# Performance work log

Measured on AMD Instinct MI355X. Metric: run time of the kernel, lower is better.

The kernel has to match this reference:

```python
import jax, jax.numpy as jnp
import numpy as np

T, B, I, H, E = 32, 128, 64, 128, 4
N_TRAP = 100  # trapezoid intervals -> 101 sample points


def setup_inputs() -> dict:
    key = jax.random.key(0)
    ks = jax.random.split(key, 14)
    s_cell = 1.0 / np.sqrt(I + H)
    s_wh = 1.0 / np.sqrt((I + H) * E)

    def u(k, shape, s):
        return jax.random.uniform(k, shape, jnp.float32, -s, s)

    return {
        "x_time": jax.random.normal(ks[0], (T, B, I), jnp.float32),
        "dt_time": jax.random.uniform(ks[1], (T, B), jnp.float32, 0.01, 1.0),
        "Wh_w": u(ks[2], ((I + H) * E, H * E), s_wh),
        "Wh_b": u(ks[3], (H * E,), s_wh),
        "Wi_w": u(ks[4], (E, I + H, H), s_cell),
        "Wi_b": u(ks[5], (E, H), s_cell),
        "Wf_w": u(ks[6], (E, I + H, H), s_cell),
        "Wf_b": u(ks[7], (E, H), s_cell),
        "Wd_w": u(ks[8], (E, I + H, H), s_cell),
        "Wd_b": u(ks[9], (E, H), s_cell),
        "Wg_w": u(ks[10], (E, I + H, H), s_cell),
        "Wg_b": u(ks[11], (E, H), s_cell),
        "Wo_w": u(ks[12], (E, I + H, H), s_cell),
        "Wo_b": u(ks[13], (E, H), s_cell),
        "alpha": jnp.ones((E, H), jnp.float32) / H,
    }


def reference(x_time, dt_time, Wh_w, Wh_b, Wi_w, Wi_b, Wf_w, Wf_b,
              Wd_w, Wd_b, Wg_w, Wg_b, Wo_w, Wo_b, alpha):
    t_total, batch, in_dim = x_time.shape
    e_types, hid = alpha.shape
    ts_unit = jnp.linspace(0.0, 1.0, N_TRAP + 1, dtype=x_time.dtype)  # [101]

    def step(carry, inp):
        h, c = carry            # each [E,B,H]
        x, dt = inp             # [B,I], [B]
        # hidden_sum = Wh(cat_m([x, h_m]))
        cat = jnp.concatenate(
            [jnp.concatenate([x, h[m]], axis=-1) for m in range(e_types)], axis=-1)  # [B,(I+H)*E]
        hs = (cat @ Wh_w + Wh_b).reshape(batch, e_types, hid).transpose(1, 0, 2)     # [E,B,H]
        iv = jnp.concatenate(
            [jnp.broadcast_to(x[None], (e_types, batch, in_dim)), hs], axis=-1)       # [E,B,I+H]

        def gate(W, b):
            return jnp.einsum('ebd,edh->ebh', iv, W) + b[:, None, :]

        i_g = jax.nn.sigmoid(gate(Wi_w, Wi_b))
        f_g = jax.nn.sigmoid(gate(Wf_w, Wf_b))
        g = f_g * c + i_g * jnp.tanh(gate(Wg_w, Wg_b))   # curr_g
        delta = jnp.exp(gate(Wd_w, Wd_b))                 # curr_delta
        o = jax.nn.sigmoid(gate(Wo_w, Wo_b))              # curr_o
        diff = c - g                                      # prev_c - curr_g

        c_new = g + diff * jnp.exp(-delta * dt[None, :, None])  # c_t at dt
        h_new = o * jnp.tanh(c_new)
        lam = jnp.einsum('eh,ebh->eb', alpha, h_new)             # intensity at dt

        # trapezoidal integration of intensity over [0, dt], 100 intervals
        ts = dt[:, None] * ts_unit                                # [B,101]
        cv = g[:, :, None, :] + diff[:, :, None, :] * jnp.exp(
            -delta[:, :, None, :] * ts[None, :, :, None])         # [E,B,101,H]
        fv = jnp.einsum('eh,ebth->ebt', alpha, o[:, :, None, :] * jnp.tanh(cv))  # [E,B,101]
        integ = (dt[None, :] / N_TRAP) * (
            jnp.sum(fv, axis=-1) - 0.5 * (fv[..., 0] + fv[..., -1]))  # [E,B]

        return (h_new, c_new), (lam.T, integ.T)  # outputs [B,E]

    h0 = jnp.zeros((e_types, batch, hid), x_time.dtype)
    c0 = jnp.zeros_like(h0)
    _, (lambdas, lambda_integrals) = jax.lax.scan(step, (h0, c0), (x_time, dt_time))
    return lambdas, lambda_integrals  # each [T,B,E]
```

## Files before the change

kernel.cpp:

```cpp
#include <hip/hip_runtime.h>

#define OFF_WALL   0
#define OFF_BIAS   196608
#define OFF_WHHH   199680
#define OFF_WGH    330752
#define OFF_XG     494592
#define OFF_GST    13077504
#define OFF_HBUF   21466112
#define GST_PLANE  2097152
#define H_SENT     0xFFFFFFFFu

typedef _Float16 half2_t __attribute__((ext_vector_type(2)));

__device__ __forceinline__ float fast_sig(float x) {
    return __fdividef(1.f, 1.f + __expf(-x));
}
__device__ __forceinline__ float sig2(float y2) {
    return __builtin_amdgcn_rcpf(exp2f(y2) + 1.f);
}
__device__ __forceinline__ unsigned pack2h(float a, float b) {
    _Float16 ha = (_Float16)a, hb = (_Float16)b;
    unsigned short ua = __builtin_bit_cast(unsigned short, ha);
    unsigned short ub = __builtin_bit_cast(unsigned short, hb);
    return ((unsigned)ub << 16) | ua;
}
__device__ __forceinline__ float dot2(unsigned w, unsigned h, float acc) {
    return __builtin_amdgcn_fdot2(__builtin_bit_cast(half2_t, w),
                                  __builtin_bit_cast(half2_t, h), acc, false);
}

__global__ __launch_bounds__(256) void k0_pack(
    const float* __restrict__ Wh_w, const float* __restrict__ Wh_b,
    const float* __restrict__ Wi_w, const float* __restrict__ Wi_b,
    const float* __restrict__ Wf_w, const float* __restrict__ Wf_b,
    const float* __restrict__ Wd_w, const float* __restrict__ Wd_b,
    const float* __restrict__ Wg_w, const float* __restrict__ Wg_b,
    const float* __restrict__ Wo_w, const float* __restrict__ Wo_b,
    float* __restrict__ ws)
{
    const float* gw[5] = {Wi_w, Wf_w, Wd_w, Wg_w, Wo_w};
    const float* gb[5] = {Wi_b, Wf_b, Wd_b, Wg_b, Wo_b};
    int idx = blockIdx.x * 256 + threadIdx.x;
    if (idx < 196608) {
        int r = idx / 3072, col = idx - r * 3072;
        float v;
        if (col < 512) {
            v = Wh_w[r * 512 + col] + Wh_w[(192 + r) * 512 + col]
              + Wh_w[(384 + r) * 512 + col] + Wh_w[(576 + r) * 512 + col];
        } else {
            int q = col - 512;
            int e = q / 640;
            int rem = q - e * 640;
            int g = rem >> 7, h = rem & 127;
            v = gw[g][(e * 192 + r) * 128 + h];
        }
        ws[OFF_WALL + idx] = v;
    } else if (idx < 327680) {
        int i = idx - 196608;
        int q    = i & 3;
        int lane = (i >> 2) & 127;
        int i4   = (i >> 9) & 15;
        int kq   = (i >> 13) & 3;
        int e    = i >> 15;
        int kp = i4 * 4 + q;
        int k0 = kq * 128 + 2 * kp;
        int r0 = (k0 >> 7) * 192 + 64 + (k0 & 127);
        float w0 = Wh_w[r0 * 512 + e * 128 + lane];
        float w1 = Wh_w[(r0 + 1) * 512 + e * 128 + lane];
        reinterpret_cast<unsigned*>(ws + OFF_WHHH)[i] = pack2h(w0, w1);
    } else if (idx < 491520) {
        int i = idx - 327680;
        int lane = i & 127;
        int gg = (i >> 7) % 5;
        int rest = (i >> 7) / 5;
        int ii = rest & 15;
        int kq = (rest >> 4) & 3;
        int e  = rest >> 6;
        int k0 = kq * 32 + 2 * ii, k1 = k0 + 1;
        float w0 = gw[gg][(e * 192 + 64 + k0) * 128 + lane];
        float w1 = gw[gg][(e * 192 + 64 + k1) * 128 + lane];
        reinterpret_cast<unsigned*>(ws + OFF_WGH)[i] = pack2h(w0, w1);
    }
    if (idx < 3072) {
        float v;
        if (idx < 512) v = Wh_b[idx];
        else {
            int q = idx - 512;
            int e = q / 640;
            int rem = q - e * 640;
            int g = rem >> 7, h = rem & 127;
            v = gb[g][e * 128 + h];
        }
        ws[OFF_BIAS + idx] = v;
    }
    if (idx < 262144) {
        reinterpret_cast<unsigned*>(ws + OFF_HBUF)[idx] = H_SENT;
    }
}

__global__ __launch_bounds__(256) void k1_xproj(
    const float* __restrict__ x, const float* wsr, float* XG)
{
    __shared__ __align__(16) float XT[64 * 68];
    const float* W_all = wsr + OFF_WALL;
    const float* bias  = wsr + OFF_BIAS;
    int bid = blockIdx.x;
    int ct = bid % 48, rt = bid / 48;
    int r0 = rt * 64, c0 = ct * 64;
    for (int p = threadIdx.x; p < 4096; p += 256) {
        int i = p >> 6, k = p & 63;
        XT[k * 68 + i] = x[(r0 + i) * 64 + k];
    }
    __syncthreads();
    int col = c0 + (threadIdx.x & 63);
    int iq = threadIdx.x >> 6;
    float acc[16];
    #pragma unroll
    for (int r = 0; r < 16; r++) acc[r] = 0.f;
    const float* wp = W_all + col;
    #pragma unroll 4
    for (int k = 0; k < 64; k++) {
        float w = wp[k * 3072];
        const float4* xt4 = reinterpret_cast<const float4*>(&XT[k * 68 + iq * 16]);
        #pragma unroll
        for (int r4 = 0; r4 < 4; r4++) {
            float4 xv = xt4[r4];
            acc[r4 * 4 + 0] = fmaf(xv.x, w, acc[r4 * 4 + 0]);
            acc[r4 * 4 + 1] = fmaf(xv.y, w, acc[r4 * 4 + 1]);
            acc[r4 * 4 + 2] = fmaf(xv.z, w, acc[r4 * 4 + 2]);
            acc[r4 * 4 + 3] = fmaf(xv.w, w, acc[r4 * 4 + 3]);
        }
    }
    float bv = bias[col];
    #pragma unroll
    for (int r = 0; r < 16; r++) {
        int row = r0 + iq * 16 + r;
        XG[row * 3072 + col] = acc[r] + bv;
    }
}

__global__ __launch_bounds__(512, 1) void k2_recur(
    const uint4* __restrict__ WhhH4,
    const unsigned* __restrict__ WgH,
    const float* __restrict__ XG,
    const float* __restrict__ dt_time,
    const float* __restrict__ alpha,
    float* __restrict__ Gst,
    unsigned* __restrict__ hbuf,
    float* __restrict__ lam_out)
{
    __shared__ __align__(16) uint4 waL[8192];
    __shared__ __align__(16) unsigned hL[256][2];
    __shared__ __align__(16) unsigned hsP[2][64];
    __shared__ __align__(16) unsigned hOut[128];
    __shared__ float pA[4][2][128];
    __shared__ __align__(16) float pBn[4][2][128][6];
    __shared__ float red[4];
    const int tid = threadIdx.x;
    const int bid = blockIdx.x;
    const int e   = (bid >> 3) & 3;
    const int grp = (bid & 7) | ((bid >> 5) << 3);
    const int b0  = grp * 2;
    const int kq  = tid >> 7;
    const int lane = tid & 127;
    const int l64 = tid & 63;
    const int s = (tid >> 7) & 1, l = lane;

    {
        const uint4* src = WhhH4 + (size_t)e * 8192;
        #pragma unroll
        for (int n = 0; n < 16; ++n) waL[tid + 512 * n] = src[tid + 512 * n];
    }
    unsigned wg[5][16];
    #pragma unroll
    for (int i = 0; i < 16; i++) {
        #pragma unroll
        for (int g = 0; g < 5; g++)
            wg[g][i] = WgH[(((e * 4 + kq) * 16 + i) * 5 + g) * 128 + lane];
    }
    const float av = alpha[e * 128 + lane];
    float cst = 0.f;
    __syncthreads();

    for (int t = 0; t < 32; ++t) {
        const int row0 = t * 128 + b0;
        float xg0 = 0.f, xgg0 = 0.f, xgg1 = 0.f, xgg2 = 0.f, xgg3 = 0.f, xgg4 = 0.f;
        if (tid < 256) {
            const float* base = XG + (size_t)(row0 + s) * 3072;
            xg0 = base[e * 128 + l];
            const float* gp = base + 512 + e * 640 + l;
            xgg0 = gp[0]; xgg1 = gp[128]; xgg2 = gp[256]; xgg3 = gp[384]; xgg4 = gp[512];
        }
        if (t > 0) {
            {
                const int eh = tid >> 7, sh = (tid >> 6) & 1, p = tid & 63;
                unsigned v;
                if (eh == e) {
                    v = hOut[tid & 127];
                } else {
                    unsigned* ap = hbuf + ((size_t)((t & 1) * 64 + grp) * 4 + e) * 512 + tid;
                    v = __hip_atomic_load(ap, __ATOMIC_RELAXED, __HIP_MEMORY_SCOPE_AGENT);
                    while (v == H_SENT) {
                        __builtin_amdgcn_s_sleep(1);
                        v = __hip_atomic_load(ap, __ATOMIC_RELAXED, __HIP_MEMORY_SCOPE_AGENT);
                    }
                    __hip_atomic_store(ap, H_SENT, __ATOMIC_RELAXED,
                                       __HIP_MEMORY_SCOPE_AGENT);
                }
                hL[eh * 64 + p][sh] = v;
            }
            __syncthreads();
            float a0 = 0.f, a1 = 0.f;
            {
                uint2 hu = reinterpret_cast<const uint2*>(hL)[kq * 64 + l64];
                #pragma unroll
                for (int i4 = 0; i4 < 16; ++i4) {
                    uint4 w = waL[(kq * 16 + i4) * 128 + lane];
                    unsigned h0, h1;
                    h0 = __builtin_amdgcn_readlane(hu.x, i4 * 4 + 0);
                    h1 = __builtin_amdgcn_readlane(hu.y, i4 * 4 + 0);
                    a0 = dot2(w.x, h0, a0); a1 = dot2(w.x, h1, a1);
                    h0 = __builtin_amdgcn_readlane(hu.x, i4 * 4 + 1);
                    h1 = __builtin_amdgcn_readlane(hu.y, i4 * 4 + 1);
                    a0 = dot2(w.y, h0, a0); a1 = dot2(w.y, h1, a1);
                    h0 = __builtin_amdgcn_readlane(hu.x, i4 * 4 + 2);
                    h1 = __builtin_amdgcn_readlane(hu.y, i4 * 4 + 2);
                    a0 = dot2(w.z, h0, a0); a1 = dot2(w.z, h1, a1);
                    h0 = __builtin_amdgcn_readlane(hu.x, i4 * 4 + 3);
                    h1 = __builtin_amdgcn_readlane(hu.y, i4 * 4 + 3);
                    a0 = dot2(w.w, h0, a0); a1 = dot2(w.w, h1, a1);
                }
            }
            pA[kq][0][lane] = a0;
            pA[kq][1][lane] = a1;
            __syncthreads();
        }
        if (tid < 256) {
            float hs = xg0;
            if (t > 0) hs += pA[0][s][l] + pA[1][s][l] + pA[2][s][l] + pA[3][s][l];
            float hi = __shfl_down(hs, 1, 64);
            if ((l & 1) == 0) hsP[s][l >> 1] = pack2h(hs, hi);
        }
        __syncthreads();
        float b0a = 0.f, b1a = 0.f, b2a = 0.f, b3a = 0.f, b4a = 0.f;
        float b0b = 0.f, b1b = 0.f, b2b = 0.f, b3b = 0.f, b4b = 0.f;
        {
            unsigned hv = hsP[(l64 >> 4) & 1][kq * 16 + (l64 & 15)];
            #pragma unroll
            for (int i = 0; i < 16; ++i) {
                unsigned h0 = __builtin_amdgcn_readlane(hv, i);
                unsigned h1 = __builtin_amdgcn_readlane(hv, 16 + i);
                b0a = dot2(wg[0][i], h0, b0a); b0b = dot2(wg[0][i], h1, b0b);
                b1a = dot2(wg[1][i], h0, b1a); b1b = dot2(wg[1][i], h1, b1b);
                b2a = dot2(wg[2][i], h0, b2a); b2b = dot2(wg[2][i], h1, b2b);
                b3a = dot2(wg[3][i], h0, b3a); b3b = dot2(wg[3][i], h1, b3b);
                b4a = dot2(wg[4][i], h0, b4a); b4b = dot2(wg[4][i], h1, b4b);
            }
        }
        {
            float2 w01, w23;
            w01.x = b0a; w01.y = b1a; w23.x = b2a; w23.y = b3a;
            *reinterpret_cast<float2*>(&pBn[kq][0][lane][0]) = w01;
            *reinterpret_cast<float2*>(&pBn[kq][0][lane][2]) = w23;
            pBn[kq][0][lane][4] = b4a;
            w01.x = b0b; w01.y = b1b; w23.x = b2b; w23.y = b3b;
            *reinterpret_cast<float2*>(&pBn[kq][1][lane][0]) = w01;
            *reinterpret_cast<float2*>(&pBn[kq][1][lane][2]) = w23;
            pBn[kq][1][lane][4] = b4b;
        }
        __syncthreads();
        if (tid < 256) {
            float ai = xgg0, af = xgg1, ad = xgg2, ag = xgg3, ao = xgg4;
            #pragma unroll
            for (int q = 0; q < 4; ++q) {
                float2 p01 = *reinterpret_cast<const float2*>(&pBn[q][s][l][0]);
                float2 p23 = *reinterpret_cast<const float2*>(&pBn[q][s][l][2]);
                float p4 = pBn[q][s][l][4];
                ai += p01.x; af += p01.y; ad += p23.x; ag += p23.y; ao += p4;
            }
            float ig = fast_sig(ai);
            float fg = fast_sig(af);
            float dl = __expf(ad);
            float gt = tanhf(ag);
            float og = fast_sig(ao);
            float gc = fmaf(fg, cst, ig * gt);
            float df = cst - gc;
            float dtv = dt_time[row0 + s];
            cst = fmaf(df, __expf(-dl * dtv), gc);
            float hn = og * tanhf(cst);
            size_t go = (size_t)(row0 + s) * 512 + e * 128 + l;
            Gst[0 * GST_PLANE + go] = gc;
            Gst[1 * GST_PLANE + go] = df;
            Gst[2 * GST_PLANE + go] = dl;
            Gst[3 * GST_PLANE + go] = og;
            float hi = __shfl_down(hn, 1, 64);
            if ((l & 1) == 0) hOut[s * 64 + (l >> 1)] = pack2h(hn, hi);
            float lm = av * hn;
            #pragma unroll
            for (int off = 32; off > 0; off >>= 1) lm += __shfl_down(lm, off, 64);
            if ((tid & 63) == 0) red[tid >> 6] = lm;
        }
        __syncthreads();
        if (tid == 0) {
            lam_out[(row0 + 0) * 4 + e] = red[0] + red[1];
            lam_out[(row0 + 1) * 4 + e] = red[2] + red[3];
        }
        {
            const int copy = tid >> 7;
            if (copy != e) {
                unsigned* dst = hbuf
                    + ((size_t)(((t + 1) & 1) * 64 + grp) * 4 + copy) * 512
                    + e * 128 + (tid & 127);
                __hip_atomic_store(dst, hOut[tid & 127], __ATOMIC_RELAXED,
                                   __HIP_MEMORY_SCOPE_AGENT);
            }
        }
    }
}

__global__ __launch_bounds__(256) void k3_trap(
    const float* __restrict__ Gst, const float* __restrict__ dt_time,
    const float* __restrict__ alpha, float* __restrict__ integ_out)
{
    __shared__ float red[4][2];
    const int row = blockIdx.x;
    const int tid = threadIdx.x;
    const float dtv = dt_time[row];
    const int base = row * 512;
    const float L2E = 1.4426950408889634f;
    float accv[2];
    #pragma unroll 1
    for (int u = 0; u < 2; ++u) {
        const int p = tid + u * 256;
        float gc = Gst[0 * GST_PLANE + base + p];
        float df = Gst[1 * GST_PLANE + base + p];
        float dl = Gst[2 * GST_PLANE + base + p];
        float o  = Gst[3 * GST_PLANE + base + p];
        float ao = alpha[p] * o;
        float G = 2.f * gc * L2E, D = 2.f * df * L2E;
        float q  = dl * dtv;
        float r1 = exp2f(-q * (0.01f * L2E));
        float r2 = r1 * r1, r4 = r2 * r2;
        float E100 = exp2f(-q * L2E);
        float sE = 0.5f * sig2(G + D) - 0.5f * sig2(fmaf(D, E100, G));
        float E1 = r1, E2 = r2, E3 = r2 * r1, E4 = r4;
        float s1 = 0.f, s2 = 0.f, s3 = 0.f, s4 = 0.f;
        #pragma unroll
        for (int k = 0; k < 25; ++k) {
            s1 += sig2(fmaf(D, E1, G)); E1 *= r4;
            s2 += sig2(fmaf(D, E2, G)); E2 *= r4;
            s3 += sig2(fmaf(D, E3, G)); E3 *= r4;
            s4 += sig2(fmaf(D, E4, G)); E4 *= r4;
        }
        sE += (s1 + s2) + (s3 + s4);
        accv[u] = ao * (100.f - 2.f * sE);
    }
    float vA = accv[0], vB = accv[1];
    #pragma unroll
    for (int off = 32; off > 0; off >>= 1) {
        vA += __shfl_down(vA, off, 64);
        vB += __shfl_down(vB, off, 64);
    }
    const int wv = tid >> 6;
    if ((tid & 63) == 0) { red[wv][0] = vA; red[wv][1] = vB; }
    __syncthreads();
    if (tid < 4) {
        float v = (tid < 2) ? (red[2 * tid][0] + red[2 * tid + 1][0])
                            : (red[2 * (tid - 2)][1] + red[2 * (tid - 2) + 1][1]);
        integ_out[row * 4 + tid] = v * (dtv * 0.01f);
    }
}

extern "C" void kernel_launch(void* const* d_in, const int* in_sizes, int n_in,
                              void* d_out, int out_size, void* d_ws, size_t ws_size,
                              hipStream_t stream)
{
    const float* x_time  = (const float*)d_in[0];
    const float* dt_time = (const float*)d_in[1];
    const float* Wh_w = (const float*)d_in[2];
    const float* Wh_b = (const float*)d_in[3];
    const float* Wi_w = (const float*)d_in[4];
    const float* Wi_b = (const float*)d_in[5];
    const float* Wf_w = (const float*)d_in[6];
    const float* Wf_b = (const float*)d_in[7];
    const float* Wd_w = (const float*)d_in[8];
    const float* Wd_b = (const float*)d_in[9];
    const float* Wg_w = (const float*)d_in[10];
    const float* Wg_b = (const float*)d_in[11];
    const float* Wo_w = (const float*)d_in[12];
    const float* Wo_b = (const float*)d_in[13];
    const float* alpha = (const float*)d_in[14];

    float* ws = (float*)d_ws;
    float* XG   = ws + OFF_XG;
    float* Gst  = ws + OFF_GST;
    unsigned* hbuf = (unsigned*)(ws + OFF_HBUF);
    float* lam_out   = (float*)d_out;
    float* integ_out = lam_out + 32 * 128 * 4;

    k0_pack<<<3072, 256, 0, stream>>>(Wh_w, Wh_b, Wi_w, Wi_b, Wf_w, Wf_b,
                                      Wd_w, Wd_b, Wg_w, Wg_b, Wo_w, Wo_b, ws);
    k1_xproj<<<3072, 256, 0, stream>>>(x_time, ws, XG);
    k2_recur<<<256, 512, 0, stream>>>(
        (const uint4*)(ws + OFF_WHHH), (const unsigned*)(ws + OFF_WGH),
        XG, dt_time, alpha, Gst, hbuf, lam_out);
    k3_trap<<<4096, 256, 0, stream>>>(Gst, dt_time, alpha, integ_out);
}
```

Before: 239.8 us.

## Load remote hidden state directly to registers with 64-bit handoff, reorganize gate reductions

In the recurrent kernel, each thread now reads its two packed h words straight from the inter-block exchange buffer as one 64-bit atomic. This drops the hL shared staging array and one block barrier per step, and the sentinel reset moves after the barrier. Producers write 64-bit packed pairs from 192 threads instead of 32-bit words. Partial gate sums move to a planar layout, and the trapezoid kernel interleaves two independent element streams with natural-exp sigmoids to raise ILP. The 64-bit sentinel check assumes a packed pair never equals all ones, and the added per-thread register pressure may cost occupancy.

Result: faster. 212.6 us (-11.3%).

```diff
diff --git a/kernel.cpp b/kernel.cpp
--- a/kernel.cpp
+++ b/kernel.cpp
@@ -8,15 +8,14 @@
 #define OFF_GST    13077504
 #define OFF_HBUF   21466112
 #define GST_PLANE  2097152
-#define H_SENT     0xFFFFFFFFu
 
 typedef _Float16 half2_t __attribute__((ext_vector_type(2)));
 
 __device__ __forceinline__ float fast_sig(float x) {
     return __fdividef(1.f, 1.f + __expf(-x));
 }
-__device__ __forceinline__ float sig2(float y2) {
-    return __builtin_amdgcn_rcpf(exp2f(y2) + 1.f);
+__device__ __forceinline__ float sig_e(float y) {
+    return __builtin_amdgcn_rcpf(__expf(y) + 1.f);
 }
 __device__ __forceinline__ unsigned pack2h(float a, float b) {
     _Float16 ha = (_Float16)a, hb = (_Float16)b;
@@ -94,7 +93,7 @@
         ws[OFF_BIAS + idx] = v;
     }
     if (idx < 262144) {
-        reinterpret_cast<unsigned*>(ws + OFF_HBUF)[idx] = H_SENT;
+        reinterpret_cast<unsigned*>(ws + OFF_HBUF)[idx] = 0xFFFFFFFFu;
     }
 }
 
@@ -150,11 +149,10 @@
     float* __restrict__ lam_out)
 {
     __shared__ __align__(16) uint4 waL[8192];
-    __shared__ __align__(16) unsigned hL[256][2];
     __shared__ __align__(16) unsigned hsP[2][64];
     __shared__ __align__(16) unsigned hOut[128];
     __shared__ float pA[4][2][128];
-    __shared__ __align__(16) float pBn[4][2][128][6];
+    __shared__ float pB[4][2][5][128];
     __shared__ float red[4];
     const int tid = threadIdx.x;
     const int bid = blockIdx.x;
@@ -192,48 +190,53 @@
             xgg0 = gp[0]; xgg1 = gp[128]; xgg2 = gp[256]; xgg3 = gp[384]; xgg4 = gp[512];
         }
         if (t > 0) {
-            {
-                const int eh = tid >> 7, sh = (tid >> 6) & 1, p = tid & 63;
-                unsigned v;
-                if (eh == e) {
-                    v = hOut[tid & 127];
-                } else {
-                    unsigned* ap = hbuf + ((size_t)((t & 1) * 64 + grp) * 4 + e) * 512 + tid;
-                    v = __hip_atomic_load(ap, __ATOMIC_RELAXED, __HIP_MEMORY_SCOPE_AGENT);
-                    while (v == H_SENT) {
-                        __builtin_amdgcn_s_sleep(1);
-                        v = __hip_atomic_load(ap, __ATOMIC_RELAXED, __HIP_MEMORY_SCOPE_AGENT);
-                    }
-                    __hip_atomic_store(ap, H_SENT, __ATOMIC_RELAXED,
-                                       __HIP_MEMORY_SCOPE_AGENT);
+            uint2 hu;
+            if (kq == e) {
+                hu.x = hOut[l64];
+                hu.y = hOut[64 + l64];
+            } else {
+                const unsigned long long* ap =
+                    reinterpret_cast<const unsigned long long*>(
+                        hbuf + ((size_t)((t & 1) * 64 + grp) * 4 + e) * 512)
+                    + (kq * 64 + l64);
+                unsigned long long v = __hip_atomic_load(ap, __ATOMIC_RELAXED,
+                                                         __HIP_MEMORY_SCOPE_AGENT);
+                while (v == ~0ull) {
+                    __builtin_amdgcn_s_sleep(1);
+                    v = __hip_atomic_load(ap, __ATOMIC_RELAXED,
+                                          __HIP_MEMORY_SCOPE_AGENT);
                 }
-                hL[eh * 64 + p][sh] = v;
+                hu.x = (unsigned)v;
+                hu.y = (unsigned)(v >> 32);
             }
-            __syncthreads();
             float a0 = 0.f, a1 = 0.f;
-            {
-                uint2 hu = reinterpret_cast<const uint2*>(hL)[kq * 64 + l64];
-                #pragma unroll
-                for (int i4 = 0; i4 < 16; ++i4) {
-                    uint4 w = waL[(kq * 16 + i4) * 128 + lane];
-                    unsigned h0, h1;
-                    h0 = __builtin_amdgcn_readlane(hu.x, i4 * 4 + 0);
-                    h1 = __builtin_amdgcn_readlane(hu.y, i4 * 4 + 0);
-                    a0 = dot2(w.x, h0, a0); a1 = dot2(w.x, h1, a1);
-                    h0 = __builtin_amdgcn_readlane(hu.x, i4 * 4 + 1);
-                    h1 = __builtin_amdgcn_readlane(hu.y, i4 * 4 + 1);
-                    a0 = dot2(w.y, h0, a0); a1 = dot2(w.y, h1, a1);
-                    h0 = __builtin_amdgcn_readlane(hu.x, i4 * 4 + 2);
-                    h1 = __builtin_amdgcn_readlane(hu.y, i4 * 4 + 2);
-                    a0 = dot2(w.z, h0, a0); a1 = dot2(w.z, h1, a1);
-                    h0 = __builtin_amdgcn_readlane(hu.x, i4 * 4 + 3);
-                    h1 = __builtin_amdgcn_readlane(hu.y, i4 * 4 + 3);
-                    a0 = dot2(w.w, h0, a0); a1 = dot2(w.w, h1, a1);
-                }
+            #pragma unroll
+            for (int i4 = 0; i4 < 16; ++i4) {
+                uint4 w = waL[(kq * 16 + i4) * 128 + lane];
+                unsigned h0, h1;
+                h0 = __builtin_amdgcn_readlane(hu.x, i4 * 4 + 0);
+                h1 = __builtin_amdgcn_readlane(hu.y, i4 * 4 + 0);
+                a0 = dot2(w.x, h0, a0); a1 = dot2(w.x, h1, a1);
+                h0 = __builtin_amdgcn_readlane(hu.x, i4 * 4 + 1);
+                h1 = __builtin_amdgcn_readlane(hu.y, i4 * 4 + 1);
+                a0 = dot2(w.y, h0, a0); a1 = dot2(w.y, h1, a1);
+                h0 = __builtin_amdgcn_readlane(hu.x, i4 * 4 + 2);
+                h1 = __builtin_amdgcn_readlane(hu.y, i4 * 4 + 2);
+                a0 = dot2(w.z, h0, a0); a1 = dot2(w.z, h1, a1);
+                h0 = __builtin_amdgcn_readlane(hu.x, i4 * 4 + 3);
+                h1 = __builtin_amdgcn_readlane(hu.y, i4 * 4 + 3);
+                a0 = dot2(w.w, h0, a0); a1 = dot2(w.w, h1, a1);
             }
             pA[kq][0][lane] = a0;
             pA[kq][1][lane] = a1;
-            __syncthreads();
+        }
+        __syncthreads();
+        if (t > 0 && kq != e && lane < 64) {
+            unsigned long long* ap =
+                reinterpret_cast<unsigned long long*>(
+                    hbuf + ((size_t)((t & 1) * 64 + grp) * 4 + e) * 512)
+                + (kq * 64 + l64);
+            __hip_atomic_store(ap, ~0ull, __ATOMIC_RELAXED, __HIP_MEMORY_SCOPE_AGENT);
         }
         if (tid < 256) {
             float hs = xg0;
@@ -257,27 +260,17 @@
                 b4a = dot2(wg[4][i], h0, b4a); b4b = dot2(wg[4][i], h1, b4b);
             }
         }
-        {
-            float2 w01, w23;
-            w01.x = b0a; w01.y = b1a; w23.x = b2a; w23.y = b3a;
-            *reinterpret_cast<float2*>(&pBn[kq][0][lane][0]) = w01;
-            *reinterpret_cast<float2*>(&pBn[kq][0][lane][2]) = w23;
-            pBn[kq][0][lane][4] = b4a;
-            w01.x = b0b; w01.y = b1b; w23.x = b2b; w23.y = b3b;
-            *reinterpret_cast<float2*>(&pBn[kq][1][lane][0]) = w01;
-            *reinterpret_cast<float2*>(&pBn[kq][1][lane][2]) = w23;
-            pBn[kq][1][lane][4] = b4b;
-        }
+        pB[kq][0][0][lane] = b0a; pB[kq][0][1][lane] = b1a; pB[kq][0][2][lane] = b2a;
+        pB[kq][0][3][lane] = b3a; pB[kq][0][4][lane] = b4a;
+        pB[kq][1][0][lane] = b0b; pB[kq][1][1][lane] = b1b; pB[kq][1][2][lane] = b2b;
+        pB[kq][1][3][lane] = b3b; pB[kq][1][4][lane] = b4b;
         __syncthreads();
         if (tid < 256) {
-            float ai = xgg0, af = xgg1, ad = xgg2, ag = xgg3, ao = xgg4;
-            #pragma unroll
-            for (int q = 0; q < 4; ++q) {
-                float2 p01 = *reinterpret_cast<const float2*>(&pBn[q][s][l][0]);
-                float2 p23 = *reinterpret_cast<const float2*>(&pBn[q][s][l][2]);
-                float p4 = pBn[q][s][l][4];
-                ai += p01.x; af += p01.y; ad += p23.x; ag += p23.y; ao += p4;
-            }
+            float ai = pB[0][s][0][l] + pB[1][s][0][l] + pB[2][s][0][l] + pB[3][s][0][l] + xgg0;
+            float af = pB[0][s][1][l] + pB[1][s][1][l] + pB[2][s][1][l] + pB[3][s][1][l] + xgg1;
+            float ad = pB[0][s][2][l] + pB[1][s][2][l] + pB[2][s][2][l] + pB[3][s][2][l] + xgg2;
+            float ag = pB[0][s][3][l] + pB[1][s][3][l] + pB[2][s][3][l] + pB[3][s][3][l] + xgg3;
+            float ao = pB[0][s][4][l] + pB[1][s][4][l] + pB[2][s][4][l] + pB[3][s][4][l] + xgg4;
             float ig = fast_sig(ai);
             float fg = fast_sig(af);
             float dl = __expf(ad);
@@ -305,15 +298,17 @@
             lam_out[(row0 + 0) * 4 + e] = red[0] + red[1];
             lam_out[(row0 + 1) * 4 + e] = red[2] + red[3];
         }
-        {
-            const int copy = tid >> 7;
-            if (copy != e) {
-                unsigned* dst = hbuf
-                    + ((size_t)(((t + 1) & 1) * 64 + grp) * 4 + copy) * 512
-                    + e * 128 + (tid & 127);
-                __hip_atomic_store(dst, hOut[tid & 127], __ATOMIC_RELAXED,
-                                   __HIP_MEMORY_SCOPE_AGENT);
-            }
+        if (tid < 192) {
+            int cpy = tid >> 6;
+            cpy += (cpy >= e) ? 1 : 0;
+            int qp = tid & 63;
+            unsigned long long v =
+                ((unsigned long long)hOut[64 + qp] << 32) | (unsigned long long)hOut[qp];
+            unsigned long long* dst =
+                reinterpret_cast<unsigned long long*>(
+                    hbuf + ((size_t)(((t + 1) & 1) * 64 + grp) * 4 + cpy) * 512)
+                + (e * 64 + qp);
+            __hip_atomic_store(dst, v, __ATOMIC_RELAXED, __HIP_MEMORY_SCOPE_AGENT);
         }
     }
 }
@@ -327,35 +322,45 @@
     const int tid = threadIdx.x;
     const float dtv = dt_time[row];
     const int base = row * 512;
-    const float L2E = 1.4426950408889634f;
-    float accv[2];
-    #pragma unroll 1
-    for (int u = 0; u < 2; ++u) {
-        const int p = tid + u * 256;
-        float gc = Gst[0 * GST_PLANE + base + p];
-        float df = Gst[1 * GST_PLANE + base + p];
-        float dl = Gst[2 * GST_PLANE + base + p];
-        float o  = Gst[3 * GST_PLANE + base + p];
-        float ao = alpha[p] * o;
-        float G = 2.f * gc * L2E, D = 2.f * df * L2E;
-        float q  = dl * dtv;
-        float r1 = exp2f(-q * (0.01f * L2E));
-        float r2 = r1 * r1, r4 = r2 * r2;
-        float E100 = exp2f(-q * L2E);
-        float sE = 0.5f * sig2(G + D) - 0.5f * sig2(fmaf(D, E100, G));
-        float E1 = r1, E2 = r2, E3 = r2 * r1, E4 = r4;
-        float s1 = 0.f, s2 = 0.f, s3 = 0.f, s4 = 0.f;
-        #pragma unroll
-        for (int k = 0; k < 25; ++k) {
-            s1 += sig2(fmaf(D, E1, G)); E1 *= r4;
-            s2 += sig2(fmaf(D, E2, G)); E2 *= r4;
-            s3 += sig2(fmaf(D, E3, G)); E3 *= r4;
-            s4 += sig2(fmaf(D, E4, G)); E4 *= r4;
-        }
-        sE += (s1 + s2) + (s3 + s4);
-        accv[u] = ao * (100.f - 2.f * sE);
-    }
-    float vA = accv[0], vB = accv[1];
+    const int iA = tid, iB = tid + 256;
+    float gcA = Gst[0 * GST_PLANE + base + iA];
+    float gcB = Gst[0 * GST_PLANE + base + iB];
+    float dfA = Gst[1 * GST_PLANE + base + iA];
+    float dfB = Gst[1 * GST_PLANE + base + iB];
+    float dlA = Gst[2 * GST_PLANE + base + iA];
+    float dlB = Gst[2 * GST_PLANE + base + iB];
+    float oA  = Gst[3 * GST_PLANE + base + iA];
+    float oB  = Gst[3 * GST_PLANE + base + iB];
+    float aoA = alpha[iA] * oA;
+    float aoB = alpha[iB] * oB;
+    float gA = 2.f * gcA, dA = 2.f * dfA;
+    float gB = 2.f * gcB, dB = 2.f * dfB;
+    float qA = dlA * dtv, qB = dlB * dtv;
+    float r1A = __expf(-qA * 0.01f), r1B = __expf(-qB * 0.01f);
+    float r2A = r1A * r1A, r2B = r1B * r1B;
+    float r4A = r2A * r2A, r4B = r2B * r2B;
+    float e100A = __expf(-qA), e100B = __expf(-qB);
+    float sA = 0.5f * sig_e(gA + dA) - 0.5f * sig_e(fmaf(dA, e100A, gA));
+    float sB = 0.5f * sig_e(gB + dB) - 0.5f * sig_e(fmaf(dB, e100B, gB));
+    float E1A = r1A, E2A = r2A, E3A = r2A * r1A, E4A = r4A;
+    float E1B = r1B, E2B = r2B, E3B = r2B * r1B, E4B = r4B;
+    float s1A = 0.f, s2A = 0.f, s3A = 0.f, s4A = 0.f;
+    float s1B = 0.f, s2B = 0.f, s3B = 0.f, s4B = 0.f;
+    #pragma unroll
+    for (int k = 0; k < 25; ++k) {
+        s1A += sig_e(fmaf(dA, E1A, gA)); E1A *= r4A;
+        s1B += sig_e(fmaf(dB, E1B, gB)); E1B *= r4B;
+        s2A += sig_e(fmaf(dA, E2A, gA)); E2A *= r4A;
+        s2B += sig_e(fmaf(dB, E2B, gB)); E2B *= r4B;
+        s3A += sig_e(fmaf(dA, E3A, gA)); E3A *= r4A;
+        s3B += sig_e(fmaf(dB, E3B, gB)); E3B *= r4B;
+        s4A += sig_e(fmaf(dA, E4A, gA)); E4A *= r4A;
+        s4B += sig_e(fmaf(dB, E4B, gB)); E4B *= r4B;
+    }
+    sA += (s1A + s2A) + (s3A + s4A);
+    sB += (s1B + s2B) + (s3B + s4B);
+    float vA = aoA * (100.f - 2.f * sA);
+    float vB = aoB * (100.f - 2.f * sB);
     #pragma unroll
     for (int off = 32; off > 0; off >>= 1) {
         vA += __shfl_down(vA, off, 64);
```
